# Kernel tuning notes

Measured on AMD Instinct MI355X. Metric: run time of the kernel, lower is better.

The kernel has to match this reference:

```python
import jax, jax.numpy as jnp
import numpy as np

B, N, L, C, H = 8, 300, 4096, 256, 8
DH = C // H  # 32; doubled to 64 after concat with pos/sine embeddings


def _linear_params(key, fan_in, fan_out):
    kw, kb = jax.random.split(key)
    bound = 1.0 / np.sqrt(fan_in)
    W = jax.random.uniform(kw, (fan_out, fan_in), jnp.float32, -bound, bound)
    b = jax.random.uniform(kb, (fan_out,), jnp.float32, -bound, bound)
    return W, b


def setup_inputs() -> dict:
    key = jax.random.key(0)
    ks = jax.random.split(key, 13)
    inp = {
        "query": jax.random.normal(ks[0], (B, N, C), jnp.float32),
        "key": jax.random.normal(ks[1], (B, L, C), jnp.float32),
        "value": jax.random.normal(ks[2], (B, L, C), jnp.float32),
        "query_pos": jax.random.normal(ks[3], (B, N, C), jnp.float32),
        "key_pos": jax.random.normal(ks[4], (B, L, C), jnp.float32),
        "query_sine_embed": jax.random.normal(ks[5], (B, N, C), jnp.float32),
    }
    names = ["qc", "qp", "qs", "kc", "kp", "v", "o"]
    for i, nm in enumerate(names):
        W, b = _linear_params(ks[6 + i], C, C)
        inp[f"W{nm}"] = W
        inp[f"b{nm}"] = b
    return inp


def reference(query, key, value, query_pos, key_pos, query_sine_embed,
              Wqc, bqc, Wqp, bqp, Wqs, bqs, Wkc, bkc, Wkp, bkp, Wv, bv, Wo, bo):
    lin = lambda x, W, b: jnp.einsum("bnc,dc->bnd", x, W) + b
    qc = lin(query, Wqc, bqc)                  # (B, N, C)
    kc = lin(key, Wkc, bkc)                    # (B, L, C)
    v = lin(value, Wv, bv)                     # (B, L, C)
    kp = lin(key_pos, Wkp, bkp)                # (B, L, C)
    qp = lin(query_pos, Wqp, bqp)              # is_first=True branch
    q = qc + qp
    k = kc + kp
    qs = lin(query_sine_embed, Wqs, bqs)
    # split heads and concat content with positional/sine embedding -> head dim 2*DH
    q = jnp.concatenate([q.reshape(B, N, H, DH), qs.reshape(B, N, H, DH)], axis=3)   # (B,N,H,2DH)
    k = jnp.concatenate([k.reshape(B, L, H, DH), kp.reshape(B, L, H, DH)], axis=3)   # (B,L,H,2DH)
    vh = v.reshape(B, L, H, DH)
    scale = (2 * DH) ** -0.5
    attn = jnp.einsum("bnhd,blhd->bhnl", q * scale, k)      # (B,H,N,L)
    attn = jax.nn.softmax(attn, axis=-1)
    out = jnp.einsum("bhnl,blhd->bnhd", attn, vh).reshape(B, N, C)
    out = jnp.einsum("bnc,dc->bnd", out, Wo) + bo
    return query + out  # identity = query
```

## Files before the change

kernel.cpp:

```cpp
#include <hip/hip_runtime.h>
#include <hip/hip_bf16.h>

using bf8_t = __attribute__((ext_vector_type(8))) short;
using bf4_t = __attribute__((ext_vector_type(4))) short;
using u16x4 = __attribute__((ext_vector_type(4))) unsigned short;
using f32x4 = __attribute__((ext_vector_type(4))) float;

constexpr int B_   = 8;
constexpr int N_   = 300;
constexpr int L_   = 4096;
constexpr int C_   = 256;
constexpr int H_   = 8;
constexpr int NPAD = 320;
constexpr int QT_  = 5;
constexpr int SPL_ = 4;
constexpr int TPS_ = 16;
constexpr float SCALE = 0.18033688011112042f;

__device__ __forceinline__ unsigned short f2b(float f) {
  unsigned u = __float_as_uint(f);
  u += 0x7FFFu + ((u >> 16) & 1u);
  return (unsigned short)(u >> 16);
}

__device__ __forceinline__ void stage_cvt16(unsigned short* dst, const float* src) {
#pragma unroll
  for (int half = 0; half < 2; ++half) {
    f32x4 x0 = *(const f32x4*)(src + half * 8);
    f32x4 x1 = *(const f32x4*)(src + half * 8 + 4);
    bf8_t v;
#pragma unroll
    for (int j = 0; j < 4; ++j) { v[j] = (short)f2b(x0[j]); v[4 + j] = (short)f2b(x1[j]); }
    *(bf8_t*)(dst + half * 8) = v;
  }
}

__device__ __forceinline__ void gload_lds16(const void* g, void* l) {
  __builtin_amdgcn_global_load_lds(
      (const __attribute__((address_space(1))) unsigned int*)g,
      (__attribute__((address_space(3))) unsigned int*)l, 16, 0, 0);
}

__device__ __forceinline__ unsigned cvt_pk_bf16(float lo, float hi) {
  unsigned r;
  asm("v_cvt_pk_bf16_f32 %0, %1, %2" : "=v"(r) : "v"(lo), "v"(hi));
  return r;
}

__global__ __launch_bounds__(256) void wcvt_k(
    const float* __restrict__ W0, const float* __restrict__ W1, const float* __restrict__ W2,
    unsigned short* __restrict__ Wq)
{
  const float* W[3] = {W0, W1, W2};
  const int kt = blockIdx.x, i = blockIdx.y;
  const int d = threadIdx.x;
  const float* src = W[i] + (size_t)d * C_ + kt * 64;
  unsigned short* dst = Wq + ((size_t)(i * 4 + kt) * 256 + d) * 64;
#pragma unroll
  for (int g = 0; g < 8; ++g) {
    f32x4 a = *(const f32x4*)(src + g * 8);
    f32x4 b = *(const f32x4*)(src + g * 8 + 4);
    bf8_t v;
#pragma unroll
    for (int j = 0; j < 4; ++j) { v[j] = (short)f2b(a[j]); v[4 + j] = (short)f2b(b[j]); }
    *(bf8_t*)(dst + (g ^ (d & 7)) * 8) = v;
  }
}

__global__ __launch_bounds__(256) void wcvt2_k(
    const float* __restrict__ W0, const float* __restrict__ W1, const float* __restrict__ W2,
    unsigned short* __restrict__ Wk)
{
  const float* W[3] = {W0, W1, W2};
  const int kt = blockIdx.x, i = blockIdx.y;
  const int d = threadIdx.x;
  const float* src = W[i] + (size_t)d * C_ + kt * 32;
  unsigned short* dst = Wk + ((size_t)(i * 8 + kt) * 256 + d) * 32;
#pragma unroll
  for (int g = 0; g < 4; ++g) {
    f32x4 a = *(const f32x4*)(src + g * 8);
    f32x4 b = *(const f32x4*)(src + g * 8 + 4);
    bf8_t v;
#pragma unroll
    for (int j = 0; j < 4; ++j) { v[j] = (short)f2b(a[j]); v[4 + j] = (short)f2b(b[j]); }
    *(bf8_t*)(dst + (g ^ (d & 3)) * 8) = v;
  }
}

__global__ __launch_bounds__(256, 4) void kvproj_k(
    const float* __restrict__ xp, const float* __restrict__ xk, const float* __restrict__ xv,
    const unsigned short* __restrict__ Wk,
    const float* __restrict__ bkp, const float* __restrict__ bkc, const float* __restrict__ bv,
    unsigned short* __restrict__ Kc, unsigned short* __restrict__ Kp, unsigned short* __restrict__ Vt)
{
  __shared__ __align__(16) unsigned short LB[20480];
  const int tid = threadIdx.x, lane = tid & 63, wv = tid >> 6;
  const int fr = lane & 15, fg = lane >> 4;
  const int i = blockIdx.y;
  const int row0 = blockIdx.x * 64;
  const int b = row0 >> 12, ll0 = row0 & (L_ - 1);
  const float* X    = (i == 0) ? xp  : (i == 1) ? xk  : xv;
  const float* bias = (i == 0) ? bkp : (i == 1) ? bkc : bv;

  const int ar = tid >> 2, ac = tid & 3;
  const int agx = (ac ^ (ar & 3)) * 8;

  f32x4 acc[4][4] = {};

  const unsigned short* Wi = Wk + (size_t)i * 8 * 8192;

  auto stageB = [&](int step, int buf) {
    const char* src = (const char*)(Wi + step * 8192);
    char* dst = (char*)(LB + 4096 + buf * 8192);
#pragma unroll
    for (int c = 0; c < 4; ++c) {
      const int off = c * 4096 + tid * 16;
      gload_lds16(src + off, dst + off);
    }
  };
  auto stageA_load = [&](int step, f32x4* arg) {
    const float* s = X + (size_t)(row0 + ar) * C_ + step * 32 + ac * 8;
    arg[0] = *(const f32x4*)s;
    arg[1] = *(const f32x4*)(s + 4);
  };
  auto stageA_write = [&](int buf, const f32x4* arg) {
    bf8_t v;
#pragma unroll
    for (int j = 0; j < 4; ++j) { v[j] = (short)f2b(arg[0][j]); v[4 + j] = (short)f2b(arg[1][j]); }
    *(bf8_t*)(LB + buf * 2048 + ar * 32 + agx) = v;
  };

  {
    f32x4 a0[2];
    stageA_load(0, a0);
    stageB(0, 0);
    stageA_write(0, a0);
  }
  __syncthreads();

  int cur = 0;
  const int gx = (fg ^ (fr & 3)) * 8;
  for (int step = 0; step < 8; ++step) {
    const int nxt = cur ^ 1;
    f32x4 arn[2];
    if (step < 7) {
      stageA_load(step + 1, arn);
      stageB(step + 1, nxt);
    }
    const unsigned short* Ab = LB + cur * 2048;
    const unsigned short* Bb = LB + 4096 + cur * 8192;
    bf8_t xf[4];
#pragma unroll
    for (int mt = 0; mt < 4; ++mt)
      xf[mt] = *(const bf8_t*)(Ab + (mt * 16 + fr) * 32 + gx);
#pragma unroll
    for (int nt = 0; nt < 4; ++nt) {
      bf8_t wf = *(const bf8_t*)(Bb + (wv * 64 + nt * 16 + fr) * 32 + gx);
#pragma unroll
      for (int mt = 0; mt < 4; ++mt)
        acc[nt][mt] = __builtin_amdgcn_mfma_f32_16x16x32_bf16(wf, xf[mt], acc[nt][mt], 0, 0, 0);
    }
    if (step < 7) stageA_write(nxt, arn);
    __syncthreads();
    cur = nxt;
  }

  if (i < 2) {
    unsigned short* outp = (i == 0) ? Kp : Kc;
#pragma unroll
    for (int nt = 0; nt < 4; ++nt) {
      const int d0 = wv * 64 + nt * 16 + fg * 4;
      const f32x4 bb = *(const f32x4*)(bias + d0);
      const int h = d0 >> 5, dh = d0 & 31;
#pragma unroll
      for (int mt = 0; mt < 4; ++mt) {
        const int l = ll0 + mt * 16 + fr;
        u16x4 v;
#pragma unroll
        for (int r = 0; r < 4; ++r) v[r] = f2b(acc[nt][mt][r] + bb[r]);
        *(u16x4*)(outp + ((size_t)(b * H_ + h) * L_ + l) * 32 + dh) = v;
      }
    }
  } else {
    unsigned short* T = LB;
#pragma unroll
    for (int nt = 0; nt < 4; ++nt) {
      const int d0 = wv * 64 + nt * 16 + fg * 4;
      const f32x4 bb = *(const f32x4*)(bias + d0);
#pragma unroll
      for (int mt = 0; mt < 4; ++mt)
#pragma unroll
        for (int r = 0; r < 4; ++r)
          T[(d0 + r) * 68 + mt * 16 + fr] = f2b(acc[nt][mt][r] + bb[r]);
    }
    __syncthreads();
    const int d = tid;
    unsigned short* dst = Vt + ((size_t)(b * H_ + (d >> 5)) * 32 + (d & 31)) * L_ + ll0;
#pragma unroll
    for (int j = 0; j < 16; ++j)
      *(u16x4*)(dst + j * 4) = *(const u16x4*)(T + d * 68 + j * 4);
  }
}

__global__ __launch_bounds__(256, 2) void qproj_k(
    const float* __restrict__ xp, const float* __restrict__ xq, const float* __restrict__ xs,
    const unsigned short* __restrict__ Wq,
    const float* __restrict__ bqp, const float* __restrict__ bqc, const float* __restrict__ bqs,
    unsigned short* __restrict__ Qcat)
{
  __shared__ __align__(16) unsigned short Al[2][64 * 64];
  __shared__ __align__(16) unsigned short Bl[2][256 * 64];
  const int tid = threadIdx.x, lane = tid & 63, wv = tid >> 6;
  const int fr = lane & 15, fg = lane >> 4;
  const int b = blockIdx.x / 5, n0 = (blockIdx.x % 5) * 64;
  const float* Ax[3] = {xp, xq, xs};

  const int sr = tid >> 2, sc = (tid & 3) * 16;
  const int ag = sc >> 3;
  const bool arow_ok = (n0 + sr) < N_;

  f32x4 acc[16] = {};

  auto stageB = [&](int step, int buf) {
    const char* bsrc = (const char*)Wq + (size_t)step * 32768;
    char* bdst = (char*)&Bl[buf][0];
#pragma unroll
    for (int c = 0; c < 8; ++c) {
      const int off = c * 4096 + wv * 1024 + lane * 16;
      gload_lds16(bsrc + off, bdst + off);
    }
  };
  auto stageA_load = [&](int step, f32x4* ar) {
    const int i = step >> 2, kt = step & 3;
    if (arow_ok) {
      const float* src = Ax[i] + ((size_t)b * N_ + n0 + sr) * C_ + kt * 64 + sc;
#pragma unroll
      for (int j = 0; j < 4; ++j) ar[j] = *(const f32x4*)(src + j * 4);
    } else {
#pragma unroll
      for (int j = 0; j < 4; ++j) ar[j] = (f32x4){0.f, 0.f, 0.f, 0.f};
    }
  };
  auto stageA_write = [&](int buf, const f32x4* ar) {
    unsigned short* base = &Al[buf][sr * 64];
    bf8_t v0, v1;
#pragma unroll
    for (int j = 0; j < 4; ++j) {
      v0[j] = (short)f2b(ar[0][j]); v0[4 + j] = (short)f2b(ar[1][j]);
      v1[j] = (short)f2b(ar[2][j]); v1[4 + j] = (short)f2b(ar[3][j]);
    }
    *(bf8_t*)(base + ((ag ^ (sr & 7)) * 8))       = v0;
    *(bf8_t*)(base + (((ag | 1) ^ (sr & 7)) * 8)) = v1;
  };

  {
    f32x4 a0[4];
    stageA_load(0, a0);
    stageB(0, 0);
    stageA_write(0, a0);
  }
  __syncthreads();

  int cur = 0;
  const int xrow = wv * 16 + fr;
  const int n_out = n0 + wv * 16 + fr;
  const bool ok = n_out < N_;
  for (int step = 0; step < 12; ++step) {
    const int nxt = cur ^ 1;
    f32x4 arn[4];
    if (step < 11) {
      stageA_load(step + 1, arn);
      stageB(step + 1, nxt);
    }
    const unsigned short* Ab = &Al[cur][0];
    const unsigned short* Bb = &Bl[cur][0];
#pragma unroll
    for (int kh = 0; kh < 2; ++kh) {
      const int gxx = (4 * kh + fg) ^ (fr & 7);
      bf8_t xf = *(const bf8_t*)(Ab + xrow * 64 + gxx * 8);
#pragma unroll
      for (int nt = 0; nt < 16; ++nt) {
        bf8_t wf = *(const bf8_t*)(Bb + (nt * 16 + fr) * 64 + gxx * 8);
        acc[nt] = __builtin_amdgcn_mfma_f32_16x16x32_bf16(wf, xf, acc[nt], 0, 0, 0);
      }
    }
    if (step == 7 || step == 11) {
      const int off = (step == 7) ? 0 : 32;
#pragma unroll
      for (int nt = 0; nt < 16; ++nt) {
        const int d0 = nt * 16 + fg * 4;
        f32x4 bb = *(const f32x4*)(bqp + d0) + *(const f32x4*)(bqc + d0);
        if (step == 11) bb += *(const f32x4*)(bqs + d0);
        u16x4 v;
#pragma unroll
        for (int r = 0; r < 4; ++r) v[r] = ok ? f2b((acc[nt][r] + bb[r]) * SCALE) : (unsigned short)0;
        *(u16x4*)(Qcat + ((size_t)(b * H_ + (d0 >> 5)) * NPAD + n_out) * 64 + off + (d0 & 31)) = v;
      }
    }
    if (step < 11) stageA_write(nxt, arn);
    __syncthreads();
    cur = nxt;
  }
}

__global__ __launch_bounds__(256, 5) void attn_k(
    const unsigned short* __restrict__ Qcat, const unsigned short* __restrict__ Kc,
    const unsigned short* __restrict__ Kp, const unsigned short* __restrict__ Vt,
    float* __restrict__ PO, float* __restrict__ PM, float* __restrict__ PLs)
{
  __shared__ __align__(16) unsigned short Kcl[2][64 * 36];
  __shared__ __align__(16) unsigned short Kpl[2][64 * 36];
  __shared__ __align__(16) unsigned short Vp[2][32][72];
  const int x = blockIdx.x;
  const int qt = x >> 8;
  const int rem = x & 255;
  const int s = rem & (SPL_ - 1);
  const int h = (rem >> 2) & (H_ - 1);
  const int b = rem >> 5;
  const int n0 = qt * 64;
  const int tid = threadIdx.x, lane = tid & 63, wv = tid >> 6;
  const int fr = lane & 15, fg = lane >> 4;

  const unsigned short* Qb = Qcat + ((size_t)b * H_ + h) * NPAD * 64;
  bf8_t qf[2];
  {
    const int qrow = n0 + wv * 16 + fr;
    qf[0] = *(const bf8_t*)&Qb[(size_t)qrow * 64 + 8 * fg];
    qf[1] = *(const bf8_t*)&Qb[(size_t)qrow * 64 + 32 + 8 * fg];
  }
  float m_r = -1e30f, l_r = 0.f;
  f32x4 o[2] = {};

  const unsigned short* KcB = Kc + ((size_t)b * H_ + h) * L_ * 32;
  const unsigned short* KpB = Kp + ((size_t)b * H_ + h) * L_ * 32;
  const unsigned short* VB  = Vt + ((size_t)b * H_ + h) * 32 * (size_t)L_;

  const int sl = tid >> 2, sg = tid & 3;
  const int vd = tid >> 3, vc = (tid & 7) * 8;

  auto loadK = [&](int t, bf8_t* kc2, bf8_t* kp2) {
    const size_t off = ((size_t)(t * 64 + sl)) * 32 + sg * 8;
    *kc2 = *(const bf8_t*)(KcB + off);
    *kp2 = *(const bf8_t*)(KpB + off);
  };

  const int t0 = s * TPS_, t1 = t0 + TPS_;
  bf8_t kcr, kpr, vreg;
  loadK(t0, &kcr, &kpr);
  vreg = *(const bf8_t*)(VB + (size_t)vd * L_ + t0 * 64 + vc);

  int cur = 0;
  for (int t = t0; t < t1; ++t) {
    {
      unsigned short* kd = &Kcl[cur][sl * 36 + sg * 8];
      unsigned short* pd = &Kpl[cur][sl * 36 + sg * 8];
      bf4_t lo, hi;
#pragma unroll
      for (int j = 0; j < 4; ++j) { lo[j] = kcr[j]; hi[j] = kcr[4 + j]; }
      *(bf4_t*)kd = lo; *(bf4_t*)(kd + 4) = hi;
#pragma unroll
      for (int j = 0; j < 4; ++j) { lo[j] = kpr[j]; hi[j] = kpr[4 + j]; }
      *(bf4_t*)pd = lo; *(bf4_t*)(pd + 4) = hi;
      *(bf8_t*)&Vp[cur][vd][vc] = vreg;
    }
    __syncthreads();
    if (t + 1 < t1) {
      loadK(t + 1, &kcr, &kpr);
      vreg = *(const bf8_t*)(VB + (size_t)vd * L_ + (t + 1) * 64 + vc);
    }
    f32x4 sc[4] = {};
#pragma unroll
    for (int nf = 0; nf < 4; ++nf) {
      const unsigned short* pc = &Kcl[cur][(nf * 16 + fr) * 36 + 8 * fg];
      const unsigned short* pp = &Kpl[cur][(nf * 16 + fr) * 36 + 8 * fg];
      bf4_t c0 = *(const bf4_t*)pc, c1 = *(const bf4_t*)(pc + 4);
      bf4_t p0 = *(const bf4_t*)pp, p1 = *(const bf4_t*)(pp + 4);
      bf8_t kf0, kf1;
#pragma unroll
      for (int j = 0; j < 4; ++j) {
        kf0[j] = c0[j]; kf0[4 + j] = c1[j];
        kf1[j] = p0[j]; kf1[4 + j] = p1[j];
      }
      sc[nf] = __builtin_amdgcn_mfma_f32_16x16x32_bf16(kf0, qf[0], sc[nf], 0, 0, 0);
      sc[nf] = __builtin_amdgcn_mfma_f32_16x16x32_bf16(kf1, qf[1], sc[nf], 0, 0, 0);
    }
    float mx = fmaxf(fmaxf(sc[0][0], sc[0][1]), fmaxf(sc[0][2], sc[0][3]));
#pragma unroll
    for (int nf = 1; nf < 4; ++nf)
      mx = fmaxf(mx, fmaxf(fmaxf(sc[nf][0], sc[nf][1]), fmaxf(sc[nf][2], sc[nf][3])));
    mx = fmaxf(mx, __shfl_xor(mx, 16));
    mx = fmaxf(mx, __shfl_xor(mx, 32));
    if (!__all(mx <= m_r + 8.f)) {
      const float mnew = fmaxf(m_r, mx);
      const float corr = exp2f(m_r - mnew);
      l_r *= corr;
#pragma unroll
      for (int r = 0; r < 4; ++r) { o[0][r] *= corr; o[1][r] *= corr; }
      m_r = mnew;
    }
    float ps = 0.f;
#pragma unroll
    for (int nf = 0; nf < 4; ++nf)
#pragma unroll
      for (int r = 0; r < 4; ++r) {
        const float p = exp2f(sc[nf][r] - m_r);
        sc[nf][r] = p;
        ps += p;
      }
    ps += __shfl_xor(ps, 16);
    ps += __shfl_xor(ps, 32);
    l_r += ps;
    unsigned pw[8];
#pragma unroll
    for (int nf = 0; nf < 4; ++nf) {
      pw[2 * nf]     = cvt_pk_bf16(sc[nf][0], sc[nf][1]);
      pw[2 * nf + 1] = cvt_pk_bf16(sc[nf][2], sc[nf][3]);
    }
#pragma unroll
    for (int kh = 0; kh < 2; ++kh) {
      union { unsigned u[4]; bf8_t v; } pu;
      pu.u[0] = pw[4 * kh];     pu.u[1] = pw[4 * kh + 1];
      pu.u[2] = pw[4 * kh + 2]; pu.u[3] = pw[4 * kh + 3];
      const bf8_t pf = pu.v;
#pragma unroll
      for (int df = 0; df < 2; ++df) {
        const unsigned short* vrow = &Vp[cur][df * 16 + fr][0];
        bf4_t va = *(const bf4_t*)(vrow + kh * 32 + fg * 4);
        bf4_t vb = *(const bf4_t*)(vrow + kh * 32 + 16 + fg * 4);
        bf8_t vf;
#pragma unroll
        for (int j = 0; j < 4; ++j) { vf[j] = va[j]; vf[4 + j] = vb[j]; }
        o[df] = __builtin_amdgcn_mfma_f32_16x16x32_bf16(vf, pf, o[df], 0, 0, 0);
      }
    }
    cur ^= 1;
  }
  const int rec = (((b * H_) + h) * QT_ + qt) * SPL_ + s;
  const int q = wv * 16 + fr;
  if (fg == 0) {
    PM [rec * 64 + q] = m_r;
    PLs[rec * 64 + q] = l_r;
  }
#pragma unroll
  for (int df = 0; df < 2; ++df)
    *(f32x4*)(PO + ((size_t)rec * 64 + q) * 32 + df * 16 + fg * 4) = o[df];
}

__global__ __launch_bounds__(256) void combine_k(
    const float* __restrict__ PO, const float* __restrict__ PM, const float* __restrict__ PLs,
    unsigned short* __restrict__ aout)
{
  const int qt = blockIdx.x, h = blockIdx.y, b = blockIdx.z;
  const int tid = threadIdx.x;
  const int row = tid >> 2, dh0 = (tid & 3) * 8;
  const int rec0 = (((b * H_) + h) * QT_ + qt) * SPL_;
  float m[SPL_], w[SPL_];
  float M = -1e30f;
#pragma unroll
  for (int s = 0; s < SPL_; ++s) { m[s] = PM[(rec0 + s) * 64 + row]; M = fmaxf(M, m[s]); }
  float denom = 0.f;
#pragma unroll
  for (int s = 0; s < SPL_; ++s) {
    w[s] = exp2f(m[s] - M);
    denom += w[s] * PLs[(rec0 + s) * 64 + row];
  }
  float num[8] = {};
#pragma unroll
  for (int s = 0; s < SPL_; ++s) {
    const float* po = PO + ((size_t)(rec0 + s) * 64 + row) * 32 + dh0;
    f32x4 a = *(const f32x4*)po;
    f32x4 c = *(const f32x4*)(po + 4);
#pragma unroll
    for (int j = 0; j < 4; ++j) { num[j] += w[s] * a[j]; num[4 + j] += w[s] * c[j]; }
  }
  const int n = qt * 64 + row;
  if (n < N_) {
    const float inv = 1.f / denom;
    bf8_t v;
#pragma unroll
    for (int j = 0; j < 8; ++j) v[j] = (short)f2b(num[j] * inv);
    *(bf8_t*)(aout + ((size_t)b * NPAD + n) * C_ + h * 32 + dh0) = v;
  }
}

__global__ __launch_bounds__(256) void oproj_k(
    const unsigned short* __restrict__ aout, const float* __restrict__ Wo,
    const float* __restrict__ bo, const float* __restrict__ query,
    float* __restrict__ out)
{
  __shared__ __align__(16) unsigned short Al[64][72];
  __shared__ __align__(16) unsigned short Bl[64][72];
  const int b = blockIdx.z, n0 = blockIdx.y * 64, d0 = blockIdx.x * 64;
  const int tid = threadIdx.x, lane = tid & 63, wv = tid >> 6;
  const int wm = wv >> 1, wn = wv & 1;
  const int sr = tid >> 2, sc = (tid & 3) * 16;
  const int fr = lane & 15, fg = lane >> 4;
  f32x4 acc[2][2] = {};

  for (int kt = 0; kt < 4; ++kt) {
    const int k0 = kt * 64;
    {
      const unsigned short* src = aout + ((size_t)b * NPAD + n0 + sr) * C_ + k0 + sc;
      *(bf8_t*)&Al[sr][sc]     = *(const bf8_t*)src;
      *(bf8_t*)&Al[sr][sc + 8] = *(const bf8_t*)(src + 8);
    }
    stage_cvt16(&Bl[sr][sc], Wo + (size_t)(d0 + sr) * C_ + k0 + sc);
    __syncthreads();
#pragma unroll
    for (int kh = 0; kh < 2; ++kh) {
      const int ko = kh * 32 + 8 * fg;
      bf8_t af[2], bq[2];
#pragma unroll
      for (int m = 0; m < 2; ++m) {
        af[m] = *(const bf8_t*)&Al[wm * 32 + m * 16 + fr][ko];
        bq[m] = *(const bf8_t*)&Bl[wn * 32 + m * 16 + fr][ko];
      }
#pragma unroll
      for (int m = 0; m < 2; ++m)
#pragma unroll
        for (int n = 0; n < 2; ++n)
          acc[m][n] = __builtin_amdgcn_mfma_f32_16x16x32_bf16(af[m], bq[n], acc[m][n], 0, 0, 0);
    }
    __syncthreads();
  }
#pragma unroll
  for (int m = 0; m < 2; ++m)
#pragma unroll
    for (int nn = 0; nn < 2; ++nn) {
      const int d = d0 + wn * 32 + nn * 16 + fr;
      const float bb = bo[d];
#pragma unroll
      for (int r = 0; r < 4; ++r) {
        const int n = n0 + wm * 32 + m * 16 + fg * 4 + r;
        if (n < N_) {
          const size_t gi = ((size_t)b * N_ + n) * C_ + d;
          out[gi] = acc[m][nn][r] + bb + query[gi];
        }
      }
    }
}

extern "C" void kernel_launch(void* const* d_in, const int* in_sizes, int n_in,
                              void* d_out, int out_size, void* d_ws, size_t ws_size,
                              hipStream_t stream)
{
  const float* query = (const float*)d_in[0];
  const float* key   = (const float*)d_in[1];
  const float* value = (const float*)d_in[2];
  const float* qpos  = (const float*)d_in[3];
  const float* kpos  = (const float*)d_in[4];
  const float* qsine = (const float*)d_in[5];
  const float* Wqc = (const float*)d_in[6];  const float* bqc = (const float*)d_in[7];
  const float* Wqp = (const float*)d_in[8];  const float* bqp = (const float*)d_in[9];
  const float* Wqs = (const float*)d_in[10]; const float* bqs = (const float*)d_in[11];
  const float* Wkc = (const float*)d_in[12]; const float* bkc = (const float*)d_in[13];
  const float* Wkp = (const float*)d_in[14]; const float* bkp = (const float*)d_in[15];
  const float* Wv  = (const float*)d_in[16]; const float* bv  = (const float*)d_in[17];
  const float* Wo  = (const float*)d_in[18]; const float* bo  = (const float*)d_in[19];

  const size_t qcat_b = (size_t)B_ * H_ * NPAD * 64 * 2;
  const size_t kc_b   = (size_t)B_ * H_ * L_ * 32 * 2;
  const size_t kp_b   = kc_b;
  const size_t vt_b   = kc_b;
  const size_t aout_b = (size_t)B_ * NPAD * C_ * 2;
  const size_t nrec   = (size_t)B_ * H_ * QT_ * SPL_;
  const size_t po_b   = nrec * 64 * 32 * 4;
  const size_t pm_b   = nrec * 64 * 4;
  const size_t pl_b   = nrec * 64 * 4;
  const size_t wsw_b  = (size_t)24 * 256 * 64 * 2;
  if (ws_size < qcat_b + kc_b + kp_b + vt_b + aout_b + po_b + pm_b + pl_b + wsw_b) return;
  char* ws = (char*)d_ws;
  unsigned short* Qcat = (unsigned short*)(ws);
  unsigned short* Kc   = (unsigned short*)(ws + qcat_b);
  unsigned short* Kp   = (unsigned short*)(ws + qcat_b + kc_b);
  unsigned short* Vt   = (unsigned short*)(ws + qcat_b + kc_b + kp_b);
  unsigned short* aout = (unsigned short*)(ws + qcat_b + kc_b + kp_b + vt_b);
  float* PO  = (float*)(ws + qcat_b + kc_b + kp_b + vt_b + aout_b);
  float* PM  = (float*)(ws + qcat_b + kc_b + kp_b + vt_b + aout_b + po_b);
  float* PLs = (float*)(ws + qcat_b + kc_b + kp_b + vt_b + aout_b + po_b + pm_b);
  unsigned short* Wq = (unsigned short*)(ws + qcat_b + kc_b + kp_b + vt_b + aout_b + po_b + pm_b + pl_b);
  unsigned short* Wk = Wq + (size_t)12 * 16384;
  float* out = (float*)d_out;

  wcvt_k   <<<dim3(4, 3),                 256, 0, stream>>>(Wqp, Wqc, Wqs, Wq);
  wcvt2_k  <<<dim3(8, 3),                 256, 0, stream>>>(Wkp, Wkc, Wv, Wk);
  qproj_k  <<<dim3(B_ * QT_),             256, 0, stream>>>(qpos, query, qsine, Wq, bqp, bqc, bqs, Qcat);
  kvproj_k <<<dim3(512, 3),               256, 0, stream>>>(kpos, key, value, Wk, bkp, bkc, bv, Kc, Kp, Vt);
  attn_k   <<<dim3(QT_ * SPL_ * B_ * H_), 256, 0, stream>>>(Qcat, Kc, Kp, Vt, PO, PM, PLs);
  combine_k<<<dim3(QT_, 8, 8),            256, 0, stream>>>(PO, PM, PLs, aout);
  oproj_k  <<<dim3(4, QT_, 8),            256, 0, stream>>>(aout, Wo, bo, query, out);
}
```

Baseline: 128.2 us.

## Split K/V projection into single-wave blocks per 64-column slice, dropping barriers

The K/V projection kernel now runs one 64-thread wave per block. Each block computes a 64-row by 64-output-column tile, and the output columns are split across a new grid z dimension, so there are four times as many blocks. With a single wave, all __syncthreads barriers are removed, and the next stage's loads are issued after the current LDS fragments are read. The trade-off is that each block loads the activation rows itself, so the same X tile is re-read and re-converted by four blocks, which multiplies input traffic and conversion work.

Result: slower. 170.3 us (+32.8%).

```diff
diff --git a/kernel.cpp b/kernel.cpp
--- a/kernel.cpp
+++ b/kernel.cpp
@@ -87,81 +87,77 @@
   }
 }
 
-__global__ __launch_bounds__(256, 4) void kvproj_k(
+__global__ __launch_bounds__(64, 2) void kvproj_k(
     const float* __restrict__ xp, const float* __restrict__ xk, const float* __restrict__ xv,
     const unsigned short* __restrict__ Wk,
     const float* __restrict__ bkp, const float* __restrict__ bkc, const float* __restrict__ bv,
     unsigned short* __restrict__ Kc, unsigned short* __restrict__ Kp, unsigned short* __restrict__ Vt)
 {
-  __shared__ __align__(16) unsigned short LB[20480];
-  const int tid = threadIdx.x, lane = tid & 63, wv = tid >> 6;
+  __shared__ __align__(16) unsigned short LB[8192];
+  const int lane = threadIdx.x;
   const int fr = lane & 15, fg = lane >> 4;
-  const int i = blockIdx.y;
+  const int i = blockIdx.y, z = blockIdx.z;
   const int row0 = blockIdx.x * 64;
   const int b = row0 >> 12, ll0 = row0 & (L_ - 1);
+  const int c0 = z * 64;
   const float* X    = (i == 0) ? xp  : (i == 1) ? xk  : xv;
   const float* bias = (i == 0) ? bkp : (i == 1) ? bkc : bv;
 
-  const int ar = tid >> 2, ac = tid & 3;
-  const int agx = (ac ^ (ar & 3)) * 8;
-
   f32x4 acc[4][4] = {};
 
-  const unsigned short* Wi = Wk + (size_t)i * 8 * 8192;
-
-  auto stageB = [&](int step, int buf) {
-    const char* src = (const char*)(Wi + step * 8192);
-    char* dst = (char*)(LB + 4096 + buf * 8192);
-#pragma unroll
-    for (int c = 0; c < 4; ++c) {
-      const int off = c * 4096 + tid * 16;
-      gload_lds16(src + off, dst + off);
-    }
-  };
-  auto stageA_load = [&](int step, f32x4* arg) {
-    const float* s = X + (size_t)(row0 + ar) * C_ + step * 32 + ac * 8;
-    arg[0] = *(const f32x4*)s;
-    arg[1] = *(const f32x4*)(s + 4);
-  };
-  auto stageA_write = [&](int buf, const f32x4* arg) {
-    bf8_t v;
-#pragma unroll
-    for (int j = 0; j < 4; ++j) { v[j] = (short)f2b(arg[0][j]); v[4 + j] = (short)f2b(arg[1][j]); }
-    *(bf8_t*)(LB + buf * 2048 + ar * 32 + agx) = v;
+  auto stageB = [&](int t, int buf) {
+    const char* src = (const char*)(Wk + ((size_t)(i * 8 + t) * 256 + c0) * 32);
+    char* dst = (char*)(LB + 4096 + buf * 2048);
+#pragma unroll
+    for (int c = 0; c < 4; ++c)
+      gload_lds16(src + c * 1024 + lane * 16, dst + c * 1024 + lane * 16);
+  };
+  auto stageA_load = [&](int t, f32x4* a) {
+    const float* s = X + (size_t)(row0 + lane) * C_ + t * 32;
+#pragma unroll
+    for (int j = 0; j < 8; ++j) a[j] = *(const f32x4*)(s + j * 4);
+  };
+  auto stageA_write = [&](int buf, const f32x4* a) {
+    unsigned short* base = LB + buf * 2048 + lane * 32;
+#pragma unroll
+    for (int j = 0; j < 4; ++j) {
+      bf8_t v;
+#pragma unroll
+      for (int q = 0; q < 4; ++q) { v[q] = (short)f2b(a[2 * j][q]); v[4 + q] = (short)f2b(a[2 * j + 1][q]); }
+      *(bf8_t*)(base + ((j ^ (lane & 3)) * 8)) = v;
+    }
   };
 
   {
-    f32x4 a0[2];
+    f32x4 a0[8];
     stageA_load(0, a0);
     stageB(0, 0);
     stageA_write(0, a0);
   }
-  __syncthreads();
 
   int cur = 0;
   const int gx = (fg ^ (fr & 3)) * 8;
-  for (int step = 0; step < 8; ++step) {
+#pragma clang loop unroll(disable)
+  for (int t = 0; t < 8; ++t) {
     const int nxt = cur ^ 1;
-    f32x4 arn[2];
-    if (step < 7) {
-      stageA_load(step + 1, arn);
-      stageB(step + 1, nxt);
-    }
     const unsigned short* Ab = LB + cur * 2048;
-    const unsigned short* Bb = LB + 4096 + cur * 8192;
-    bf8_t xf[4];
-#pragma unroll
-    for (int mt = 0; mt < 4; ++mt)
-      xf[mt] = *(const bf8_t*)(Ab + (mt * 16 + fr) * 32 + gx);
-#pragma unroll
-    for (int nt = 0; nt < 4; ++nt) {
-      bf8_t wf = *(const bf8_t*)(Bb + (wv * 64 + nt * 16 + fr) * 32 + gx);
+    const unsigned short* Bb = LB + 4096 + cur * 2048;
+    bf8_t xf[4], wf[4];
+#pragma unroll
+    for (int mt = 0; mt < 4; ++mt) xf[mt] = *(const bf8_t*)(Ab + (mt * 16 + fr) * 32 + gx);
+#pragma unroll
+    for (int nt = 0; nt < 4; ++nt) wf[nt] = *(const bf8_t*)(Bb + (nt * 16 + fr) * 32 + gx);
+    f32x4 an[8];
+    if (t < 7) {
+      stageA_load(t + 1, an);
+      stageB(t + 1, nxt);
+    }
+#pragma unroll
+    for (int nt = 0; nt < 4; ++nt)
 #pragma unroll
       for (int mt = 0; mt < 4; ++mt)
-        acc[nt][mt] = __builtin_amdgcn_mfma_f32_16x16x32_bf16(wf, xf[mt], acc[nt][mt], 0, 0, 0);
-    }
-    if (step < 7) stageA_write(nxt, arn);
-    __syncthreads();
+        acc[nt][mt] = __builtin_amdgcn_mfma_f32_16x16x32_bf16(wf[nt], xf[mt], acc[nt][mt], 0, 0, 0);
+    if (t < 7) stageA_write(nxt, an);
     cur = nxt;
   }
 
@@ -169,7 +165,7 @@
     unsigned short* outp = (i == 0) ? Kp : Kc;
 #pragma unroll
     for (int nt = 0; nt < 4; ++nt) {
-      const int d0 = wv * 64 + nt * 16 + fg * 4;
+      const int d0 = c0 + nt * 16 + fg * 4;
       const f32x4 bb = *(const f32x4*)(bias + d0);
       const int h = d0 >> 5, dh = d0 & 31;
 #pragma unroll
@@ -185,20 +181,20 @@
     unsigned short* T = LB;
 #pragma unroll
     for (int nt = 0; nt < 4; ++nt) {
-      const int d0 = wv * 64 + nt * 16 + fg * 4;
+      const int d0 = c0 + nt * 16 + fg * 4;
       const f32x4 bb = *(const f32x4*)(bias + d0);
+      const int dl0 = nt * 16 + fg * 4;
 #pragma unroll
       for (int mt = 0; mt < 4; ++mt)
 #pragma unroll
         for (int r = 0; r < 4; ++r)
-          T[(d0 + r) * 68 + mt * 16 + fr] = f2b(acc[nt][mt][r] + bb[r]);
-    }
-    __syncthreads();
-    const int d = tid;
+          T[(dl0 + r) * 68 + mt * 16 + fr] = f2b(acc[nt][mt][r] + bb[r]);
+    }
+    const int d = c0 + lane;
     unsigned short* dst = Vt + ((size_t)(b * H_ + (d >> 5)) * 32 + (d & 31)) * L_ + ll0;
 #pragma unroll
     for (int j = 0; j < 16; ++j)
-      *(u16x4*)(dst + j * 4) = *(const u16x4*)(T + d * 68 + j * 4);
+      *(u16x4*)(dst + j * 4) = *(const u16x4*)(T + lane * 68 + j * 4);
   }
 }
 
@@ -585,7 +581,7 @@
   wcvt_k   <<<dim3(4, 3),                 256, 0, stream>>>(Wqp, Wqc, Wqs, Wq);
   wcvt2_k  <<<dim3(8, 3),                 256, 0, stream>>>(Wkp, Wkc, Wv, Wk);
   qproj_k  <<<dim3(B_ * QT_),             256, 0, stream>>>(qpos, query, qsine, Wq, bqp, bqc, bqs, Qcat);
-  kvproj_k <<<dim3(512, 3),               256, 0, stream>>>(kpos, key, value, Wk, bkp, bkc, bv, Kc, Kp, Vt);
+  kvproj_k <<<dim3(512, 3, 4),            64,  0, stream>>>(kpos, key, value, Wk, bkp, bkc, bv, Kc, Kp, Vt);
   attn_k   <<<dim3(QT_ * SPL_ * B_ * H_), 256, 0, stream>>>(Qcat, Kc, Kp, Vt, PO, PM, PLs);
   combine_k<<<dim3(QT_, 8, 8),            256, 0, stream>>>(PO, PM, PLs, aout);
   oproj_k  <<<dim3(4, QT_, 8),            256, 0, stream>>>(aout, Wo, bo, query, out);
```
